# Optimization experiments

Hardware: AMD Instinct MI355X
Metric: run time of the kernel (lower is better)

Reference implementation:

```python
import jax, jax.numpy as jnp
import numpy as np

M, K, N = 32, 4096, 12288


def setup_inputs() -> dict:
    key = jax.random.key(0)
    k1, k2, k3, k4 = jax.random.split(key, 4)
    x = jax.random.normal(k1, (M, K), dtype=jnp.float32)
    # uint8-valued packed weight (stored as int32 for harness compatibility, values in [0,256))
    weight_u8 = jax.random.randint(k2, (K, N), 0, 256, dtype=jnp.int32)
    # per-output-channel fp16 scale and zero-point
    scale = (jax.random.uniform(k3, (N,), dtype=jnp.float32) * 0.01 + 1e-3).astype(jnp.float16)
    zero = (jax.random.uniform(k4, (N,), dtype=jnp.float32) * 255.0).astype(jnp.float16)
    return {"x": x, "weight_u8": weight_u8, "scale": scale, "zero": zero}


def reference(x, weight_u8, scale, zero):
    # QuantMatmulCustom: dequantize uint8 weight with per-channel fp16 scale/zero, then matmul.
    # w_deq[k, n] = (w_u8[k, n] - zero[n]) * scale[n]
    w_deq = (weight_u8.astype(jnp.float32) - zero.astype(jnp.float32)[None, :]) * scale.astype(jnp.float32)[None, :]
    # [M, K] @ [K, N] -> [M, N]
    return jnp.einsum('mk,kn->mn', x, w_deq)
```

## Files before the change

### kernel.cpp

```cpp
#include <hip/hip_runtime.h>

#define M_DIM 32
#define K_DIM 4096
#define N_DIM 12288
#define SPLITK 16
#define KPER  (K_DIM / SPLITK)
#define NT    (KPER / 32)
#define BLK   512
#define NPB   128

using bf16x8 = __attribute__((ext_vector_type(8))) short;
using f32x4  = __attribute__((ext_vector_type(4))) float;

typedef __attribute__((address_space(1))) const void GASV;
typedef __attribute__((address_space(3))) void LASV;

__device__ __forceinline__ bf16x8 pack_b(const int (&wv)[8]) {
    bf16x8 b;
    #pragma unroll
    for (int j = 0; j < 8; ++j) {
        float f = (float)wv[j];
        b[j] = (short)(__float_as_uint(f) >> 16);
    }
    return b;
}

template <bool WS>
__global__ __launch_bounds__(BLK, 4) void qmm_main(const float* __restrict__ x,
                                                   const int* __restrict__ w,
                                                   float* __restrict__ dst) {
    __shared__ short lds_a[NT * 2 * 64 * 8];
    __shared__ int   lds_b[2][32 * 128];

    const int tid  = threadIdx.x;
    const int lane = tid & 63;
    const int g    = lane >> 4;
    const int c    = lane & 15;
    const int wid  = tid >> 6;
    const int k0   = blockIdx.y * KPER;
    const int n0   = blockIdx.x * NPB;
    const int n0w  = n0 + wid * 16;

    const int* gsrc[2];
    #pragma unroll
    for (int q = 0; q < 2; ++q) {
        const int i     = wid * 2 + q;
        const int r     = 2 * i + (lane >> 5);
        const int nslot = 4 * (lane & 31);
        const int col   = nslot ^ (((r >> 3) & 1) << 4);
        gsrc[q] = w + (size_t)(k0 + r) * N_DIM + n0 + col;
    }

    #pragma unroll
    for (int q = 0; q < 2; ++q) {
        __builtin_amdgcn_global_load_lds((GASV*)gsrc[q],
                                         (LASV*)&lds_b[0][(wid * 2 + q) * 256], 16, 0, 0);
        __builtin_amdgcn_global_load_lds((GASV*)(gsrc[q] + (size_t)32 * N_DIM),
                                         (LASV*)&lds_b[1][(wid * 2 + q) * 256], 16, 0, 0);
    }

    for (int s = tid; s < NT * 2 * 64; s += BLK) {
        const int l  = s & 63;
        const int h  = (s >> 6) & 1;
        const int kt = s >> 7;
        const int m  = 16 * h + (l & 15);
        const float* xp = x + (size_t)m * K_DIM + k0 + kt * 32 + 8 * (l >> 4);
        bf16x8 v;
        #pragma unroll
        for (int j = 0; j < 8; ++j) {
            unsigned u = __float_as_uint(xp[j]);
            u += 0x7FFFu + ((u >> 16) & 1u);
            v[j] = (short)(u >> 16);
        }
        *(bf16x8*)&lds_a[s * 8] = v;
    }
    __syncthreads();

    f32x4 acc0 = {0.f, 0.f, 0.f, 0.f};
    f32x4 acc1 = {0.f, 0.f, 0.f, 0.f};

    const short* la     = lds_a + lane * 8;
    const int    colrd  = (wid * 16 + c) ^ ((g & 1) << 4);

    #pragma unroll
    for (int t = 0; t < NT; ++t) {
        const int* bb = &lds_b[t & 1][g * 8 * 128 + colrd];
        int wv[8];
        #pragma unroll
        for (int j = 0; j < 8; ++j) wv[j] = bb[j * 128];
        bf16x8 bf = pack_b(wv);
        bf16x8 a0 = *(const bf16x8*)&la[(size_t)(t * 2 + 0) * 512];
        bf16x8 a1 = *(const bf16x8*)&la[(size_t)(t * 2 + 1) * 512];
        acc0 = __builtin_amdgcn_mfma_f32_16x16x32_bf16(a0, bf, acc0, 0, 0, 0);
        acc1 = __builtin_amdgcn_mfma_f32_16x16x32_bf16(a1, bf, acc1, 0, 0, 0);

        __syncthreads();
        if (t + 2 < NT) {
            #pragma unroll
            for (int q = 0; q < 2; ++q)
                __builtin_amdgcn_global_load_lds(
                    (GASV*)(gsrc[q] + (size_t)32 * (t + 2) * N_DIM),
                    (LASV*)&lds_b[t & 1][(wid * 2 + q) * 256], 16, 0, 0);
        }
    }

    if (WS) {
        float* pp = dst + ((size_t)blockIdx.y * M_DIM) * N_DIM + n0w + c;
        #pragma unroll
        for (int i = 0; i < 4; ++i) {
            const int r = 4 * (lane >> 4) + i;
            pp[(size_t)r * N_DIM]        = acc0[i];
            pp[(size_t)(16 + r) * N_DIM] = acc1[i];
        }
    } else {
        #pragma unroll
        for (int i = 0; i < 4; ++i) {
            const int r = 4 * (lane >> 4) + i;
            atomicAdd(&dst[(size_t)r * N_DIM + n0w + c], acc0[i]);
            atomicAdd(&dst[(size_t)(16 + r) * N_DIM + n0w + c], acc1[i]);
        }
    }
}

__global__ __launch_bounds__(256) void qmm_rowsum(const float* __restrict__ x,
                                                  float* __restrict__ rowsum) {
    const int m = blockIdx.x;
    __shared__ float red[256];
    const float4* xp = (const float4*)(x + (size_t)m * K_DIM);
    float s = 0.f;
    #pragma unroll
    for (int i = 0; i < K_DIM / 4 / 256; ++i) {
        float4 v = xp[threadIdx.x + 256 * i];
        s += v.x + v.y + v.z + v.w;
    }
    red[threadIdx.x] = s;
    __syncthreads();
    #pragma unroll
    for (int off = 128; off > 0; off >>= 1) {
        if (threadIdx.x < off) red[threadIdx.x] += red[threadIdx.x + off];
        __syncthreads();
    }
    if (threadIdx.x == 0) rowsum[m] = red[0];
}

__global__ __launch_bounds__(256) void qmm_finalize(const float* __restrict__ part,
                                                    const float* __restrict__ rowsum,
                                                    const float* __restrict__ scale,
                                                    const float* __restrict__ zero,
                                                    float* __restrict__ out) {
    const int m  = blockIdx.y;
    const int n4 = blockIdx.x * 256 + threadIdx.x;
    const float rs = rowsum[m];
    float4 acc = make_float4(0.f, 0.f, 0.f, 0.f);
    #pragma unroll
    for (int sp = 0; sp < SPLITK; ++sp) {
        float4 p = ((const float4*)(part + ((size_t)sp * M_DIM + m) * N_DIM))[n4];
        acc.x += p.x; acc.y += p.y; acc.z += p.z; acc.w += p.w;
    }
    const float4 sc = ((const float4*)scale)[n4];
    const float4 zp = ((const float4*)zero)[n4];
    float4 o;
    o.x = sc.x * (acc.x - zp.x * rs);
    o.y = sc.y * (acc.y - zp.y * rs);
    o.z = sc.z * (acc.z - zp.z * rs);
    o.w = sc.w * (acc.w - zp.w * rs);
    ((float4*)(out + (size_t)m * N_DIM))[n4] = o;
}

__global__ __launch_bounds__(256) void qmm_zero(float* __restrict__ out) {
    int i = blockIdx.x * 256 + threadIdx.x;
    ((float4*)out)[i] = make_float4(0.f, 0.f, 0.f, 0.f);
}
__global__ __launch_bounds__(256) void qmm_scale(const float* __restrict__ x,
                                                 const float* __restrict__ scale,
                                                 const float* __restrict__ zero,
                                                 float* __restrict__ out) {
    const int m = blockIdx.y;
    __shared__ float red[256];
    float s = 0.f;
    for (int k = threadIdx.x; k < K_DIM; k += 256)
        s += x[(size_t)m * K_DIM + k];
    red[threadIdx.x] = s;
    __syncthreads();
    #pragma unroll
    for (int off = 128; off > 0; off >>= 1) {
        if (threadIdx.x < off) red[threadIdx.x] += red[threadIdx.x + off];
        __syncthreads();
    }
    const float rowsum = red[0];
    const int n = blockIdx.x * 256 + threadIdx.x;
    const float v = out[(size_t)m * N_DIM + n];
    out[(size_t)m * N_DIM + n] = scale[n] * (v - zero[n] * rowsum);
}

extern "C" void kernel_launch(void* const* d_in, const int* in_sizes, int n_in,
                              void* d_out, int out_size, void* d_ws, size_t ws_size,
                              hipStream_t stream) {
    const float* x     = (const float*)d_in[0];
    const int*   w     = (const int*)d_in[1];
    const float* scale = (const float*)d_in[2];
    const float* zero  = (const float*)d_in[3];
    float* out = (float*)d_out;

    const size_t part_sz = (size_t)SPLITK * M_DIM * N_DIM * sizeof(float);
    const size_t need    = part_sz + M_DIM * sizeof(float);
    if (ws_size >= need) {
        float* part   = (float*)d_ws;
        float* rowsum = (float*)((char*)d_ws + part_sz);
        qmm_main<true><<<dim3(N_DIM / NPB, SPLITK), dim3(BLK), 0, stream>>>(x, w, part);
        qmm_rowsum    <<<dim3(M_DIM),               dim3(256), 0, stream>>>(x, rowsum);
        qmm_finalize  <<<dim3(N_DIM / 4 / 256, M_DIM), dim3(256), 0, stream>>>(part, rowsum, scale, zero, out);
    } else {
        qmm_zero <<<dim3((M_DIM * N_DIM / 4) / 256),  dim3(256), 0, stream>>>(out);
        qmm_main<false><<<dim3(N_DIM / NPB, SPLITK),  dim3(BLK), 0, stream>>>(x, w, out);
        qmm_scale<<<dim3(N_DIM / 256, M_DIM),         dim3(256), 0, stream>>>(x, scale, zero, out);
    }
}
```

Before: 45.99 us.

## Use per-wave 4-deep LDS pipeline with vmcnt waits instead of block barriers

Each wave now loads only its own 16-column slice of the weight tile into a private 4-slot LDS ring and issues loads four k-steps ahead. It waits on specific vmcnt counts instead of calling __syncthreads every iteration, which is meant to remove block-wide barrier stalls and keep more global loads in flight. The A operand is preloaded into registers, and the int-to-bf16 packing uses v_perm to combine pairs of values. The trade-offs are higher register use and a fully unrolled schedule that depends on manual waitcnt correctness, with possible read/DMA-write hazards on LDS slot reuse.

```diff
diff --git a/kernel.cpp b/kernel.cpp
--- a/kernel.cpp
+++ b/kernel.cpp
@@ -8,6 +8,7 @@
 #define NT    (KPER / 32)
 #define BLK   512
 #define NPB   128
+#define DBUF  4
 
 using bf16x8 = __attribute__((ext_vector_type(8))) short;
 using f32x4  = __attribute__((ext_vector_type(4))) float;
@@ -16,13 +17,14 @@
 typedef __attribute__((address_space(3))) void LASV;
 
 __device__ __forceinline__ bf16x8 pack_b(const int (&wv)[8]) {
-    bf16x8 b;
-    #pragma unroll
-    for (int j = 0; j < 8; ++j) {
-        float f = (float)wv[j];
-        b[j] = (short)(__float_as_uint(f) >> 16);
-    }
-    return b;
+    union { unsigned u[4]; bf16x8 v; } r;
+    #pragma unroll
+    for (int p = 0; p < 4; ++p) {
+        unsigned a = __float_as_uint((float)wv[2 * p]);
+        unsigned b = __float_as_uint((float)wv[2 * p + 1]);
+        r.u[p] = __builtin_amdgcn_perm(b, a, 0x07060302);
+    }
+    return r.v;
 }
 
 template <bool WS>
@@ -30,7 +32,7 @@
                                                    const int* __restrict__ w,
                                                    float* __restrict__ dst) {
     __shared__ short lds_a[NT * 2 * 64 * 8];
-    __shared__ int   lds_b[2][32 * 128];
+    __shared__ int   lds_b[8 * DBUF * 512];
 
     const int tid  = threadIdx.x;
     const int lane = tid & 63;
@@ -44,20 +46,24 @@
     const int* gsrc[2];
     #pragma unroll
     for (int q = 0; q < 2; ++q) {
-        const int i     = wid * 2 + q;
-        const int r     = 2 * i + (lane >> 5);
-        const int nslot = 4 * (lane & 31);
-        const int col   = nslot ^ (((r >> 3) & 1) << 4);
-        gsrc[q] = w + (size_t)(k0 + r) * N_DIM + n0 + col;
-    }
-
-    #pragma unroll
-    for (int q = 0; q < 2; ++q) {
-        __builtin_amdgcn_global_load_lds((GASV*)gsrc[q],
-                                         (LASV*)&lds_b[0][(wid * 2 + q) * 256], 16, 0, 0);
-        __builtin_amdgcn_global_load_lds((GASV*)(gsrc[q] + (size_t)32 * N_DIM),
-                                         (LASV*)&lds_b[1][(wid * 2 + q) * 256], 16, 0, 0);
-    }
+        const int r  = 16 * q + (lane >> 2);
+        const int cg = (lane & 3) ^ ((r >> 3) & 3);
+        gsrc[q] = w + (size_t)(k0 + r) * N_DIM + n0w + 4 * cg;
+    }
+    int* const ldst = &lds_b[wid * (DBUF * 512)];
+
+#define ISSUE(T) do {                                                          \
+    __builtin_amdgcn_sched_barrier(0);                                         \
+    __builtin_amdgcn_global_load_lds((GASV*)(gsrc[0] + (size_t)32 * (T) * N_DIM), \
+        (LASV*)(ldst + ((T) & 3) * 512),       16, 0, 0);                      \
+    __builtin_amdgcn_global_load_lds((GASV*)(gsrc[1] + (size_t)32 * (T) * N_DIM), \
+        (LASV*)(ldst + ((T) & 3) * 512 + 256), 16, 0, 0);                      \
+} while (0)
+
+#define WAITV(N) do { asm volatile("s_waitcnt vmcnt(" #N ")" ::: "memory");    \
+    __builtin_amdgcn_sched_barrier(0); } while (0)
+
+    ISSUE(0); ISSUE(1); ISSUE(2); ISSUE(3);
 
     for (int s = tid; s < NT * 2 * 64; s += BLK) {
         const int l  = s & 63;
@@ -76,33 +82,40 @@
     }
     __syncthreads();
 
+    bf16x8 areg[NT * 2];
+    {
+        const short* la = lds_a + lane * 8;
+        #pragma unroll
+        for (int i = 0; i < NT * 2; ++i)
+            areg[i] = *(const bf16x8*)&la[(size_t)i * 512];
+    }
+
+    const int* brd = lds_b + wid * (DBUF * 512) + 128 * g + 4 * ((c >> 2) ^ g) + (c & 3);
+
     f32x4 acc0 = {0.f, 0.f, 0.f, 0.f};
     f32x4 acc1 = {0.f, 0.f, 0.f, 0.f};
 
-    const short* la     = lds_a + lane * 8;
-    const int    colrd  = (wid * 16 + c) ^ ((g & 1) << 4);
-
-    #pragma unroll
-    for (int t = 0; t < NT; ++t) {
-        const int* bb = &lds_b[t & 1][g * 8 * 128 + colrd];
-        int wv[8];
-        #pragma unroll
-        for (int j = 0; j < 8; ++j) wv[j] = bb[j * 128];
-        bf16x8 bf = pack_b(wv);
-        bf16x8 a0 = *(const bf16x8*)&la[(size_t)(t * 2 + 0) * 512];
-        bf16x8 a1 = *(const bf16x8*)&la[(size_t)(t * 2 + 1) * 512];
-        acc0 = __builtin_amdgcn_mfma_f32_16x16x32_bf16(a0, bf, acc0, 0, 0, 0);
-        acc1 = __builtin_amdgcn_mfma_f32_16x16x32_bf16(a1, bf, acc1, 0, 0, 0);
-
-        __syncthreads();
-        if (t + 2 < NT) {
-            #pragma unroll
-            for (int q = 0; q < 2; ++q)
-                __builtin_amdgcn_global_load_lds(
-                    (GASV*)(gsrc[q] + (size_t)32 * (t + 2) * N_DIM),
-                    (LASV*)&lds_b[t & 1][(wid * 2 + q) * 256], 16, 0, 0);
-        }
-    }
+#define COMP(T) do {                                                           \
+    int wv[8];                                                                 \
+    _Pragma("unroll")                                                          \
+    for (int j = 0; j < 8; ++j) wv[j] = brd[((T) & 3) * 512 + j * 16];         \
+    bf16x8 bfv = pack_b(wv);                                                   \
+    acc0 = __builtin_amdgcn_mfma_f32_16x16x32_bf16(areg[2*(T)],   bfv, acc0, 0, 0, 0); \
+    acc1 = __builtin_amdgcn_mfma_f32_16x16x32_bf16(areg[2*(T)+1], bfv, acc1, 0, 0, 0); \
+} while (0)
+
+    COMP(0); ISSUE(4);
+    COMP(1); ISSUE(5);
+    COMP(2); ISSUE(6);
+    COMP(3); ISSUE(7);
+    WAITV(6); COMP(4);
+    WAITV(4); COMP(5);
+    WAITV(2); COMP(6);
+    WAITV(0); COMP(7);
+
+#undef ISSUE
+#undef WAITV
+#undef COMP
 
     if (WS) {
         float* pp = dst + ((size_t)blockIdx.y * M_DIM) * N_DIM + n0w + c;
```

Measured after the change: 45.73 us. Within noise of the previous version (-0.6%).
